# Kernel optimization log

Measured on AMD Instinct MI355X. Metric: run time of the kernel, lower is better.

## Reference

```python
import jax, jax.numpy as jnp
import numpy as np

N, D = 4096, 512
W_L2, W_TOPO = 1.0, 1.0
BIG = jnp.float32(1e30)


def setup_inputs() -> dict:
    key = jax.random.key(0)
    k1, k2 = jax.random.split(key)
    x_1 = jax.random.normal(k1, (N, D), dtype=jnp.float32)
    x_2 = jax.random.normal(k2, (N, D), dtype=jnp.float32)
    return {"x_1": x_1, "x_2": x_2}


def _pdist(x):
    # Euclidean pairwise distances [n, n]; diagonal set to BIG so it is never
    # selected as an MST edge and sqrt(0) never appears in the grad path.
    sq = jnp.sum(x * x, axis=1)
    d2 = sq[:, None] + sq[None, :] - 2.0 * (x @ x.T)
    d2 = jnp.maximum(d2, 1e-12)
    n = x.shape[0]
    d2 = jnp.where(jnp.eye(n, dtype=bool), BIG, d2)
    return jnp.sqrt(d2)


def _h0_deaths(dist):
    # H0 persistence of the Vietoris-Rips filtration == MST edge weights
    # (births are all 0). Prim's algorithm via lax.scan, O(n^2).
    n = dist.shape[0]
    in_tree0 = jnp.zeros(n, dtype=bool).at[0].set(True)

    def step(carry, _):
        min_dist, in_tree = carry  # min_dist[k] = min edge from tree to k
        md = jnp.where(in_tree, BIG, min_dist)
        j = jnp.argmin(md)
        w = md[j]  # weight of the MST edge added this step = an H0 death
        min_dist = jnp.minimum(min_dist, dist[j])
        in_tree = in_tree.at[j].set(True)
        return (min_dist, in_tree), w

    (_, _), deaths = jax.lax.scan(step, (dist[0], in_tree0), None, length=n - 1)
    return deaths  # [n-1]


def _wasserstein1(d1, d2):
    # 1-Wasserstein between two H0 diagrams {(0, death_i)} with L_inf ground
    # metric and diagonal projections allowed. Equal-cardinality diagrams on
    # the birth=0 axis: match sorted deaths, per-pair cost is the cheaper of
    # direct matching |a-b| or routing both points to the diagonal (a+b)/2.
    a = jnp.sort(d1)
    b = jnp.sort(d2)
    cost = jnp.minimum(jnp.abs(a - b), 0.5 * (a + b))
    return jnp.sum(cost)


def reference(x_1, x_2):
    representation_loss = jnp.mean((x_1 - x_2) ** 2)
    deaths_1 = _h0_deaths(_pdist(x_1))
    deaths_2 = _h0_deaths(_pdist(x_2))
    topological_loss = _wasserstein1(deaths_1, deaths_2)
    return W_L2 * representation_loss + W_TOPO * topological_loss
```

## Files before the change

### kernel.cpp

```cpp
#include <hip/hip_runtime.h>

#define N 4096
#define D 512
#define BIG 1e30f
#define CMAX 2048
#define CMAX2 1024
#define CMAX3 512
#define NW (N / 32)

typedef unsigned long long u64;
typedef unsigned short u16;
typedef _Float16 f16x8 __attribute__((ext_vector_type(8)));
typedef float floatx4 __attribute__((ext_vector_type(4)));

__global__ __launch_bounds__(256) void prep_kernel(const float* __restrict__ x1,
                                                   const float* __restrict__ x2,
                                                   u16* __restrict__ h1,
                                                   u16* __restrict__ h2,
                                                   float* __restrict__ sq,
                                                   float* __restrict__ accumArr,
                                                   int* __restrict__ comp,
                                                   u64* __restrict__ compBest,
                                                   int* __restrict__ comp_c,
                                                   int* __restrict__ doneFlag) {
    const int tid = blockIdx.x * 256 + threadIdx.x;
    if (tid < 2 * N) {
        comp[tid] = tid & (N - 1);
        compBest[tid] = ~0ull;
    }
    if (tid < 2 * CMAX) comp_c[tid] = tid & (CMAX - 1);
    if (tid == 0) doneFlag[0] = 0;

    const int wave = threadIdx.x >> 6, lane = threadIdx.x & 63;
    const int row = blockIdx.x * 4 + wave;
    const float4* r1 = (const float4*)(x1 + (size_t)row * D);
    const float4* r2 = (const float4*)(x2 + (size_t)row * D);
    float4 a0 = r1[lane * 2], a1 = r1[lane * 2 + 1];
    float4 b0 = r2[lane * 2], b1 = r2[lane * 2 + 1];
    ushort4* o1 = (ushort4*)(h1 + (size_t)row * D + lane * 8);
    ushort4* o2 = (ushort4*)(h2 + (size_t)row * D + lane * 8);
    o1[0] = make_ushort4(__builtin_bit_cast(u16, (_Float16)a0.x), __builtin_bit_cast(u16, (_Float16)a0.y),
                         __builtin_bit_cast(u16, (_Float16)a0.z), __builtin_bit_cast(u16, (_Float16)a0.w));
    o1[1] = make_ushort4(__builtin_bit_cast(u16, (_Float16)a1.x), __builtin_bit_cast(u16, (_Float16)a1.y),
                         __builtin_bit_cast(u16, (_Float16)a1.z), __builtin_bit_cast(u16, (_Float16)a1.w));
    o2[0] = make_ushort4(__builtin_bit_cast(u16, (_Float16)b0.x), __builtin_bit_cast(u16, (_Float16)b0.y),
                         __builtin_bit_cast(u16, (_Float16)b0.z), __builtin_bit_cast(u16, (_Float16)b0.w));
    o2[1] = make_ushort4(__builtin_bit_cast(u16, (_Float16)b1.x), __builtin_bit_cast(u16, (_Float16)b1.y),
                         __builtin_bit_cast(u16, (_Float16)b1.z), __builtin_bit_cast(u16, (_Float16)b1.w));
    float s1 = 0.f, s2 = 0.f, sr = 0.f;
    float av[8] = {a0.x, a0.y, a0.z, a0.w, a1.x, a1.y, a1.z, a1.w};
    float bv[8] = {b0.x, b0.y, b0.z, b0.w, b1.x, b1.y, b1.z, b1.w};
#pragma unroll
    for (int e = 0; e < 8; ++e) {
        s1 = fmaf(av[e], av[e], s1);
        s2 = fmaf(bv[e], bv[e], s2);
        float d = av[e] - bv[e];
        sr = fmaf(d, d, sr);
    }
#pragma unroll
    for (int off = 32; off > 0; off >>= 1) {
        s1 += __shfl_down(s1, off, 64);
        s2 += __shfl_down(s2, off, 64);
        sr += __shfl_down(sr, off, 64);
    }
    __shared__ float wsr[4];
    if (lane == 0) {
        sq[row] = s1;
        sq[N + row] = s2;
        wsr[wave] = sr;
    }
    __syncthreads();
    if (threadIdx.x == 0)
        accumArr[blockIdx.x] = wsr[0] + wsr[1] + wsr[2] + wsr[3];
}

#define BM 128
#define BN 128
#define BK 32
#define NB (N / BM)
#define NPAIR (NB * (NB + 1) / 2)
#define NT (D / BK)

__global__ __launch_bounds__(256) void gemm_dist_sym_kernel(const u16* __restrict__ h1,
                                                            const u16* __restrict__ h2,
                                                            const float* __restrict__ sqn,
                                                            float* __restrict__ dist1,
                                                            float* __restrict__ dist2,
                                                            u64* __restrict__ compBest) {
    const int m = blockIdx.z;
    const u16* H = m ? h2 : h1;
    const float* SQ = sqn + (size_t)m * N;
    float* dist = m ? dist2 : dist1;
    u64* cb = compBest + (size_t)m * N;

    const int t = blockIdx.x;
    int by = (int)((65.0f - sqrtf(4225.0f - 8.0f * (float)t)) * 0.5f);
    while (by > 0 && by * 32 - by * (by - 1) / 2 > t) --by;
    while ((by + 1) * 32 - (by + 1) * by / 2 <= t) ++by;
    const int bx = by + (t - (by * 32 - by * (by - 1) / 2));
    const bool diag = (by == bx);

    __shared__ u16 SH[4 * BM * BK];
    u16* A0 = SH;
    u16* B0 = SH + BM * BK;
    u16* A1 = SH + 2 * BM * BK;
    u16* B1 = SH + 3 * BM * BK;

    const int tid = threadIdx.x;
    const int wave = tid >> 6, lane = tid & 63;
    const int wm = wave >> 1, wn = wave & 1;
    const int row0 = by * BM, col0 = bx * BN;

    floatx4 acc[4][4] = {};

    const int srow = lane >> 2;
    const int scol = (lane & 3) * 8;

#define STAGE(AB, BB, K0)                                                                      \
    {                                                                                          \
        _Pragma("unroll") for (int i_ = 0; i_ < 2; ++i_) {                                     \
            const int rb_ = wave * 32 + i_ * 16;                                               \
            const u16* ga_ = H + (size_t)(row0 + rb_ + srow) * D + (K0) + scol;                \
            __builtin_amdgcn_global_load_lds(                                                  \
                (const __attribute__((address_space(1))) unsigned int*)ga_,                    \
                (__attribute__((address_space(3))) unsigned int*)&(AB)[rb_ * BK], 16, 0, 0);   \
            if (!diag) {                                                                       \
                const u16* gb_ = H + (size_t)(col0 + rb_ + srow) * D + (K0) + scol;            \
                __builtin_amdgcn_global_load_lds(                                              \
                    (const __attribute__((address_space(1))) unsigned int*)gb_,                \
                    (__attribute__((address_space(3))) unsigned int*)&(BB)[rb_ * BK], 16, 0, 0); \
            }                                                                                  \
        }                                                                                      \
    }

    STAGE(A0, B0, 0);
    __syncthreads();

    const int fo = (lane >> 4) * 8;
    const int fm = lane & 15;
#pragma unroll 2
    for (int kt = 0; kt < NT; ++kt) {
        u16* Ac = (kt & 1) ? A1 : A0;
        u16* Bc = (kt & 1) ? B1 : B0;
        if (kt + 1 < NT) {
            u16* An = (kt & 1) ? A0 : A1;
            u16* Bn = (kt & 1) ? B0 : B1;
            STAGE(An, Bn, (kt + 1) * BK);
        }
        const u16* Bs = diag ? Ac : Bc;
        f16x8 a8[4], b8[4];
#pragma unroll
        for (int s = 0; s < 4; ++s) {
            a8[s] = *(const f16x8*)&Ac[(wm * 64 + s * 16 + fm) * BK + fo];
            b8[s] = *(const f16x8*)&Bs[(wn * 64 + s * 16 + fm) * BK + fo];
        }
#pragma unroll
        for (int i = 0; i < 4; ++i)
#pragma unroll
            for (int j = 0; j < 4; ++j)
                acc[i][j] = __builtin_amdgcn_mfma_f32_16x16x32_f16(a8[i], b8[j], acc[i][j], 0, 0, 0);
        __syncthreads();
    }
#undef STAGE

    float* Cs = (float*)SH + wave * 1024;

    const int lr = lane & 15;
    const int lq = lane >> 4;
    float sc[4];
#pragma unroll
    for (int ns = 0; ns < 4; ++ns) sc[ns] = SQ[col0 + wn * 64 + ns * 16 + lr];
    u64 colBest[4] = {~0ull, ~0ull, ~0ull, ~0ull};
#pragma unroll
    for (int ms = 0; ms < 4; ++ms) {
        const int rb = row0 + wm * 64 + ms * 16 + lq * 4;
        float srow_[4];
#pragma unroll
        for (int r = 0; r < 4; ++r) srow_[r] = SQ[rb + r];
#pragma unroll
        for (int r = 0; r < 4; ++r) {
            const int row = rb + r;
            float dval[4];
#pragma unroll
            for (int ns = 0; ns < 4; ++ns) {
                const int col = col0 + wn * 64 + ns * 16 + lr;
                float d2 = srow_[r] + sc[ns] - 2.0f * acc[ms][ns][r];
                dval[ns] = (row == col) ? BIG : sqrtf(fmaxf(d2, 1e-12f));
            }
            float vmin = fminf(fminf(dval[0], dval[1]), fminf(dval[2], dval[3]));
            int nsel = (dval[0] == vmin) ? 0 : (dval[1] == vmin) ? 1 : (dval[2] == vmin) ? 2 : 3;
            u64 pmin = (((u64)__float_as_uint(vmin)) << 32) | (unsigned)(col0 + wn * 64 + nsel * 16 + lr);
#pragma unroll
            for (int msk = 1; msk < 16; msk <<= 1) {
                u64 o = __shfl_xor(pmin, msk, 64);
                pmin = o < pmin ? o : pmin;
            }
            if (lr == 0) atomicMin(&cb[row], pmin);
            if (!diag) {
#pragma unroll
                for (int ns = 0; ns < 4; ++ns) {
                    u64 p = (((u64)__float_as_uint(dval[ns])) << 32) | (unsigned)row;
                    colBest[ns] = p < colBest[ns] ? p : colBest[ns];
                }
            }
#pragma unroll
            for (int ns = 0; ns < 4; ++ns)
                Cs[(lq * 4 + r) * 64 + ns * 16 + lr] = dval[ns];
        }
#pragma unroll
        for (int p = 0; p < 4; ++p) {
            float4 v4 = *(float4*)&Cs[p * 256 + lane * 4];
            const int gr = row0 + wm * 64 + ms * 16 + p * 4 + (lane >> 4);
            const int gc = col0 + wn * 64 + (lane & 15) * 4;
            *(float4*)&dist[(size_t)gr * N + gc] = v4;
        }
    }
    if (!diag) {
#pragma unroll
        for (int ns = 0; ns < 4; ++ns) {
            u64 b = colBest[ns];
            u64 o = __shfl_xor(b, 16, 64);
            b = o < b ? o : b;
            o = __shfl_xor(b, 32, 64);
            b = o < b ? o : b;
            if (lq == 0) atomicMin(&cb[col0 + wn * 64 + ns * 16 + lr], b);
        }
    }
}

__global__ __launch_bounds__(1024) void merge1i_kernel(int* __restrict__ comp,
                                                       u64* __restrict__ compBest,
                                                       float* __restrict__ deaths,
                                                       int* __restrict__ cnt,
                                                       int* __restrict__ numComp,
                                                       int* __restrict__ numC1,
                                                       unsigned* __restrict__ distc_u) {
    const int t = threadIdx.x;
    if (blockIdx.x >= 2) {
        const size_t idx = (size_t)(blockIdx.x - 2) * 1024 + t;
        uint4 v = make_uint4(0x7f800000u, 0x7f800000u, 0x7f800000u, 0x7f800000u);
        ((uint4*)distc_u)[idx] = v;
        ((uint4*)distc_u)[idx + 1048576] = v;
        return;
    }
    const int m = blockIdx.x;
    int* cp = comp + (size_t)m * N;
    u64* cb = compBest + (size_t)m * N;
    float* dth = deaths + (size_t)m * N;

    __shared__ int pa[N];
    __shared__ int pb[N];
    __shared__ unsigned flagbits[NW];
    __shared__ int wpc[NW];
    __shared__ int done;

    if (t == 0) cnt[m] = 0;
    __syncthreads();

    for (int c = t; c < N; c += 1024) {
        u64 best = cb[c];
        int p = c;
        if (best != ~0ull) {
            int j = (int)(unsigned)best;
            int c2 = cp[j];
            u64 best2 = cb[c2];
            int j2 = (int)(unsigned)best2;
            bool mutual = (cp[j2] == c);
            if (!(mutual && c < c2)) {
                p = c2;
                int idx = atomicAdd(cnt + m, 1);
                dth[idx] = __uint_as_float((unsigned)(best >> 32));
            }
        }
        pa[c] = p;
    }

    int* A = pa;
    int* B = pb;
    while (true) {
        __syncthreads();
        if (t == 0) done = 1;
        __syncthreads();
        bool ch = false;
        for (int c = t; c < N; c += 1024) {
            int g = A[A[c]];
            B[c] = g;
            ch |= (g != A[c]);
        }
        if (ch) done = 0;
        __syncthreads();
        int* tmp = A; A = B; B = tmp;
        if (done) break;
    }

    for (int w = t; w < NW; w += 1024) flagbits[w] = 0u;
    __syncthreads();
    for (int i = t; i < N; i += 1024)
        atomicOr(&flagbits[A[i] >> 5], 1u << (A[i] & 31));
    __syncthreads();
    if (t < NW) wpc[t] = __popc(flagbits[t]);
    __syncthreads();
    for (int off = 1; off < NW; off <<= 1) {
        int v = 0;
        if (t < NW) v = wpc[t] + ((t >= off) ? wpc[t - off] : 0);
        __syncthreads();
        if (t < NW) wpc[t] = v;
        __syncthreads();
    }
    for (int i = t; i < N; i += 1024) {
        int root = A[i];
        int w = root >> 5, b = root & 31;
        int base = w ? wpc[w - 1] : 0;
        unsigned mask = b ? ((1u << b) - 1u) : 0u;
        cp[i] = base + __popc(flagbits[w] & mask);
    }
    for (int c = t; c < N; c += 1024) cb[c] = ~0ull;
    if (t == 0) {
        int C1 = wpc[NW - 1];
        numC1[m] = C1;
        numComp[m] = C1;
    }
}

__global__ __launch_bounds__(256) void rowatomic_kernel(const float* __restrict__ dist1,
                                                        const float* __restrict__ dist2,
                                                        const int* __restrict__ comp,
                                                        unsigned* __restrict__ distc_u) {
    const int m = blockIdx.y;
    const float* dist = m ? dist2 : dist1;
    const int* cp = comp + (size_t)m * N;
    const int i = blockIdx.x;
    const float4* row4 = (const float4*)(dist + (size_t)i * N);
    const int4* cp4 = (const int4*)cp;
    __shared__ unsigned bins[CMAX];
    const int t = threadIdx.x;
    for (int b = t; b < CMAX; b += 256) bins[b] = 0x7f800000u;
    __syncthreads();
    const int q0 = (i >> 7) << 5;
    for (int q = q0 + t; q < N / 4; q += 256) {
        float4 v = row4[q];
        int4 cj = cp4[q];
        atomicMin(&bins[cj.x], __float_as_uint(v.x));
        atomicMin(&bins[cj.y], __float_as_uint(v.y));
        atomicMin(&bins[cj.z], __float_as_uint(v.z));
        atomicMin(&bins[cj.w], __float_as_uint(v.w));
    }
    __syncthreads();
    unsigned* drow = distc_u + ((size_t)m * CMAX + cp[i]) * CMAX;
    for (int b = t; b < CMAX; b += 256) {
        unsigned v = bins[b];
        if (v != 0x7f800000u) atomicMin(&drow[b], v);
    }
}

#define CT 64
#define NCT (CMAX / CT)
#define NPAIRC (NCT * (NCT + 1) / 2)
__global__ __launch_bounds__(256) void symscan_kernel(unsigned* __restrict__ distc_u,
                                                      u64* __restrict__ compBest,
                                                      const int* __restrict__ numComp,
                                                      const int* __restrict__ numC1,
                                                      unsigned* __restrict__ distc2_u) {
    const int tid = threadIdx.x;
    if (blockIdx.x >= NPAIRC) {
        const size_t base = ((size_t)blockIdx.y * 256 + (blockIdx.x - NPAIRC)) * 256 + tid;
        uint4 v = make_uint4(0x7f800000u, 0x7f800000u, 0x7f800000u, 0x7f800000u);
#pragma unroll
        for (int k = 0; k < 4; ++k)
            ((uint4*)distc2_u)[base + (size_t)k * 131072] = v;
        return;
    }
    const int m = blockIdx.y;
    if (numComp[m] <= 1) return;
    const int C1 = numC1[m];
    const int t = blockIdx.x;
    int a = (int)((65.0f - sqrtf(4225.0f - 8.0f * (float)t)) * 0.5f);
    while (a > 0 && a * 32 - a * (a - 1) / 2 > t) --a;
    while ((a + 1) * 32 - (a + 1) * a / 2 <= t) ++a;
    const int b = a + (t - (a * 32 - a * (a - 1) / 2));
    if (a * CT >= C1 || b * CT >= C1) return;

    unsigned* Dm = distc_u + (size_t)m * CMAX * CMAX;
    unsigned* P = Dm + (size_t)(a * CT) * CMAX + b * CT;
    unsigned* Q = Dm + (size_t)(b * CT) * CMAX + a * CT;
    u64* cb = compBest + (size_t)m * N;

    __shared__ float L[CT][CT + 1];
    __shared__ float M[CT][CT + 1];
#pragma unroll
    for (int e0 = 0; e0 < 4; ++e0) {
        int e = e0 * 256 + tid;
        int r = e >> 4, c4 = (e & 15) << 2;
        float4 v = *(const float4*)&Q[(size_t)r * CMAX + c4];
        L[r][c4] = v.x; L[r][c4 + 1] = v.y; L[r][c4 + 2] = v.z; L[r][c4 + 3] = v.w;
    }
    __syncthreads();
#pragma unroll
    for (int e0 = 0; e0 < 4; ++e0) {
        int e = e0 * 256 + tid;
        int r = e >> 4, c4 = (e & 15) << 2;
        float4 v = *(const float4*)&P[(size_t)r * CMAX + c4];
        float4 f;
        f.x = fminf(v.x, L[c4 + 0][r]);
        f.y = fminf(v.y, L[c4 + 1][r]);
        f.z = fminf(v.z, L[c4 + 2][r]);
        f.w = fminf(v.w, L[c4 + 3][r]);
        *(float4*)&P[(size_t)r * CMAX + c4] = f;
        M[r][c4] = f.x; M[r][c4 + 1] = f.y; M[r][c4 + 2] = f.z; M[r][c4 + 3] = f.w;
    }
    __syncthreads();

    {
        const int rloc = tid >> 2;
        const int r = a * CT + rloc;
        const int c0 = (tid & 3) * 16;
        u64 best = ~0ull;
#pragma unroll
        for (int c = 0; c < 16; ++c) {
            const int j = b * CT + c0 + c;
            const unsigned bits = __float_as_uint(M[rloc][c0 + c]);
            if (j < C1 && j != r && bits < 0x7f800000u) {
                u64 p = (((u64)bits) << 32) | (unsigned)j;
                best = p < best ? p : best;
            }
        }
        u64 o = __shfl_xor(best, 1, 64); best = o < best ? o : best;
        o = __shfl_xor(best, 2, 64); best = o < best ? o : best;
        if ((tid & 3) == 0 && r < C1 && best != ~0ull) atomicMin(&cb[r], best);
    }

    if (a == b) return;

    {
        const int rloc = tid >> 2;
        const int r = b * CT + rloc;
        const int c0 = (tid & 3) * 16;
        u64 best = ~0ull;
#pragma unroll
        for (int c = 0; c < 16; ++c) {
            const int j = a * CT + c0 + c;
            const unsigned bits = __float_as_uint(M[c0 + c][rloc]);
            if (j < C1 && bits < 0x7f800000u) {
                u64 p = (((u64)bits) << 32) | (unsigned)j;
                best = p < best ? p : best;
            }
        }
        u64 o = __shfl_xor(best, 1, 64); best = o < best ? o : best;
        o = __shfl_xor(best, 2, 64); best = o < best ? o : best;
        if ((tid & 3) == 0 && r < C1 && best != ~0ull) atomicMin(&cb[r], best);
    }

#pragma unroll
    for (int e0 = 0; e0 < 4; ++e0) {
        int e = e0 * 256 + tid;
        int r = e >> 4, c4 = (e & 15) << 2;
        float4 f;
        f.x = M[c4 + 0][r];
        f.y = M[c4 + 1][r];
        f.z = M[c4 + 2][r];
        f.w = M[c4 + 3][r];
        *(float4*)&Q[(size_t)r * CMAX + c4] = f;
    }
}

__global__ __launch_bounds__(1024) void merge2_kernel(int* __restrict__ comp_c,
                                                      u64* __restrict__ compBest,
                                                      float* __restrict__ deaths,
                                                      int* __restrict__ cnt,
                                                      int* __restrict__ numComp,
                                                      const int* __restrict__ numC1,
                                                      int* __restrict__ numC2,
                                                      int* __restrict__ comp_c2) {
    const int m = blockIdx.x;
    const int t = threadIdx.x;
    const int C1 = numC1[m];
    int* cc2i = comp_c2 + (size_t)m * CMAX2;
    for (int c = t; c < CMAX2; c += 1024) cc2i[c] = c;
    if (numComp[m] <= 1) {
        if (t == 0) numC2[m] = numComp[m];
        return;
    }
    int* cc = comp_c + (size_t)m * CMAX;
    u64* cb = compBest + (size_t)m * N;
    float* dth = deaths + (size_t)m * N;

    __shared__ int pa[CMAX];
    __shared__ int pb[CMAX];
    __shared__ unsigned flagbits[CMAX / 32];
    __shared__ int wpc[CMAX / 32];
    __shared__ int done;

    for (int c = t; c < C1; c += 1024) {
        u64 best = cb[c];
        int p = c;
        if (best != ~0ull) {
            int j = (int)(unsigned)best;
            int c2 = cc[j];
            u64 best2 = cb[c2];
            int j2 = (int)(unsigned)best2;
            bool mutual = (cc[j2] == c);
            if (!(mutual && c < c2)) {
                p = c2;
                int idx = atomicAdd(cnt + m, 1);
                dth[idx] = __uint_as_float((unsigned)(best >> 32));
            }
        }
        pa[c] = p;
    }

    int* A = pa;
    int* B = pb;
    while (true) {
        __syncthreads();
        if (t == 0) done = 1;
        __syncthreads();
        bool ch = false;
        for (int c = t; c < C1; c += 1024) {
            int g = A[A[c]];
            B[c] = g;
            ch |= (g != A[c]);
        }
        if (ch) done = 0;
        __syncthreads();
        int* tmp = A; A = B; B = tmp;
        if (done) break;
    }

    for (int w = t; w < CMAX / 32; w += 1024) flagbits[w] = 0u;
    __syncthreads();
    for (int j = t; j < C1; j += 1024)
        atomicOr(&flagbits[A[j] >> 5], 1u << (A[j] & 31));
    __syncthreads();
    if (t < CMAX / 32) wpc[t] = __popc(flagbits[t]);
    __syncthreads();
    for (int off = 1; off < CMAX / 32; off <<= 1) {
        int v = 0;
        if (t < CMAX / 32) v = wpc[t] + ((t >= off) ? wpc[t - off] : 0);
        __syncthreads();
        if (t < CMAX / 32) wpc[t] = v;
        __syncthreads();
    }
    for (int j = t; j < C1; j += 1024) {
        int root = A[j];
        int w = root >> 5, b = root & 31;
        int base = w ? wpc[w - 1] : 0;
        unsigned mask = b ? ((1u << b) - 1u) : 0u;
        cc[j] = base + __popc(flagbits[w] & mask);
    }
    for (int c = t; c < C1; c += 1024) cb[c] = ~0ull;
    if (t == 0) {
        int C2 = wpc[CMAX / 32 - 1];
        numC2[m] = C2;
        numComp[m] = C2;
    }
}

__global__ __launch_bounds__(256) void rowatomic2_kernel(const float* __restrict__ distc,
                                                         const int* __restrict__ comp_c,
                                                         const int* __restrict__ numComp,
                                                         const int* __restrict__ numC1,
                                                         unsigned* __restrict__ distc2_u) {
    const int m = blockIdx.y;
    if (numComp[m] <= 1) return;
    const int C1 = numC1[m];
    const int r = blockIdx.x;
    if (r >= C1) return;
    const int* cc = comp_c + (size_t)m * CMAX;
    const float* row = distc + ((size_t)m * CMAX + r) * CMAX;
    __shared__ unsigned bins[CMAX2];
    const int t = threadIdx.x;
    for (int b = t; b < CMAX2; b += 256) bins[b] = 0x7f800000u;
    __syncthreads();
    for (int j = t; j < C1; j += 256)
        atomicMin(&bins[cc[j]], __float_as_uint(row[j]));
    __syncthreads();
    unsigned* drow = distc2_u + ((size_t)m * CMAX2 + cc[r]) * CMAX2;
    for (int b = t; b < CMAX2; b += 256) {
        unsigned v = bins[b];
        if (v != 0x7f800000u) atomicMin(&drow[b], v);
    }
}

__global__ __launch_bounds__(256) void scan3_kernel(const float* __restrict__ distc2,
                                                    const int* __restrict__ comp_c2,
                                                    u64* __restrict__ compBest,
                                                    const int* __restrict__ numComp,
                                                    const int* __restrict__ numC2,
                                                    unsigned* __restrict__ distc3_u) {
    const int t = threadIdx.x;
    if (blockIdx.x >= 2 * CMAX2) {
        const size_t idx = (size_t)(blockIdx.x - 2 * CMAX2) * 256 + t;
        uint4 v = make_uint4(0x7f800000u, 0x7f800000u, 0x7f800000u, 0x7f800000u);
        ((uint4*)distc3_u)[idx] = v;
        ((uint4*)distc3_u)[idx + 65536] = v;
        return;
    }
    const int m = blockIdx.x >> 10;
    if (numComp[m] <= 1) return;
    const int C2 = numC2[m];
    const int r = blockIdx.x & (CMAX2 - 1);
    if (r >= C2) return;
    const int* cc = comp_c2 + (size_t)m * CMAX2;
    u64* cb = compBest + (size_t)m * N;
    const int myc = cc[r];
    const float4* row4 = (const float4*)(distc2 + ((size_t)m * CMAX2 + r) * CMAX2);
    const int4* cc4 = (const int4*)cc;
    float4 v = row4[t];
    int4 cj = cc4[t];
    int j0 = t * 4;
    u64 p0 = (j0 + 0 < C2 && cj.x != myc) ? ((((u64)__float_as_uint(v.x)) << 32) | (unsigned)(j0 + 0)) : ~0ull;
    u64 p1 = (j0 + 1 < C2 && cj.y != myc) ? ((((u64)__float_as_uint(v.y)) << 32) | (unsigned)(j0 + 1)) : ~0ull;
    u64 p2 = (j0 + 2 < C2 && cj.z != myc) ? ((((u64)__float_as_uint(v.z)) << 32) | (unsigned)(j0 + 2)) : ~0ull;
    u64 p3 = (j0 + 3 < C2 && cj.w != myc) ? ((((u64)__float_as_uint(v.w)) << 32) | (unsigned)(j0 + 3)) : ~0ull;
    u64 q0 = p0 < p1 ? p0 : p1;
    u64 q1 = p2 < p3 ? p2 : p3;
    u64 best = q0 < q1 ? q0 : q1;
#pragma unroll
    for (int off = 32; off > 0; off >>= 1) {
        u64 o = __shfl_down(best, off, 64);
        best = o < best ? o : best;
    }
    if ((t & 63) == 0) atomicMin(cb + myc, best);
}

__global__ __launch_bounds__(1024) void merge3_kernel(int* __restrict__ comp_c2,
                                                      u64* __restrict__ compBest,
                                                      float* __restrict__ deaths,
                                                      int* __restrict__ cnt,
                                                      int* __restrict__ numComp,
                                                      const int* __restrict__ numC2,
                                                      int* __restrict__ numC3) {
    const int m = blockIdx.x;
    const int t = threadIdx.x;
    if (numComp[m] <= 1) {
        if (t == 0) numC3[m] = numComp[m];
        return;
    }
    const int C2 = numC2[m];
    int* cc = comp_c2 + (size_t)m * CMAX2;
    u64* cb = compBest + (size_t)m * N;
    float* dth = deaths + (size_t)m * N;

    __shared__ int pa[CMAX2];
    __shared__ int pb[CMAX2];
    __shared__ unsigned flagbits[CMAX2 / 32];
    __shared__ int wpc[CMAX2 / 32];
    __shared__ int done;

    for (int c = t; c < C2; c += 1024) {
        u64 best = cb[c];
        int p = c;
        if (best != ~0ull) {
            int j = (int)(unsigned)best;
            int c2 = cc[j];
            u64 best2 = cb[c2];
            int j2 = (int)(unsigned)best2;
            bool mutual = (cc[j2] == c);
            if (!(mutual && c < c2)) {
                p = c2;
                int idx = atomicAdd(cnt + m, 1);
                dth[idx] = __uint_as_float((unsigned)(best >> 32));
            }
        }
        pa[c] = p;
    }

    int* A = pa;
    int* B = pb;
    while (true) {
        __syncthreads();
        if (t == 0) done = 1;
        __syncthreads();
        bool ch = false;
        for (int c = t; c < C2; c += 1024) {
            int g = A[A[c]];
            B[c] = g;
            ch |= (g != A[c]);
        }
        if (ch) done = 0;
        __syncthreads();
        int* tmp = A; A = B; B = tmp;
        if (done) break;
    }

    for (int w = t; w < CMAX2 / 32; w += 1024) flagbits[w] = 0u;
    __syncthreads();
    for (int j = t; j < C2; j += 1024)
        atomicOr(&flagbits[A[j] >> 5], 1u << (A[j] & 31));
    __syncthreads();
    if (t < CMAX2 / 32) wpc[t] = __popc(flagbits[t]);
    __syncthreads();
    for (int off = 1; off < CMAX2 / 32; off <<= 1) {
        int v = 0;
        if (t < CMAX2 / 32) v = wpc[t] + ((t >= off) ? wpc[t - off] : 0);
        __syncthreads();
        if (t < CMAX2 / 32) wpc[t] = v;
        __syncthreads();
    }
    for (int j = t; j < C2; j += 1024) {
        int root = A[j];
        int w = root >> 5, b = root & 31;
        int base = w ? wpc[w - 1] : 0;
        unsigned mask = b ? ((1u << b) - 1u) : 0u;
        cc[j] = base + __popc(flagbits[w] & mask);
    }
    for (int c = t; c < C2; c += 1024) cb[c] = ~0ull;
    if (t == 0) {
        int C3 = wpc[CMAX2 / 32 - 1];
        numC3[m] = C3;
        numComp[m] = C3;
    }
}

__global__ __launch_bounds__(256) void rowatomic3_kernel(const float* __restrict__ distc2,
                                                         const int* __restrict__ comp_c2,
                                                         const int* __restrict__ numComp,
                                                         const int* __restrict__ numC2,
                                                         unsigned* __restrict__ distc3_u) {
    const int m = blockIdx.y;
    if (numComp[m] <= 1) return;
    const int C2 = numC2[m];
    const int r = blockIdx.x;
    if (r >= C2) return;
    const int* cc = comp_c2 + (size_t)m * CMAX2;
    const float* row = distc2 + ((size_t)m * CMAX2 + r) * CMAX2;
    __shared__ unsigned bins[CMAX3];
    const int t = threadIdx.x;
    for (int b = t; b < CMAX3; b += 256) bins[b] = 0x7f800000u;
    __syncthreads();
    for (int j = t; j < C2; j += 256)
        atomicMin(&bins[cc[j]], __float_as_uint(row[j]));
    __syncthreads();
    unsigned* drow = distc3_u + ((size_t)m * CMAX3 + cc[r]) * CMAX3;
    for (int b = t; b < CMAX3; b += 256) {
        unsigned v = bins[b];
        if (v != 0x7f800000u) atomicMin(&drow[b], v);
    }
}

__global__ __launch_bounds__(1024) void finish_kernel(const float* __restrict__ distc3,
                                                      float* __restrict__ deaths,
                                                      int* __restrict__ cnt,
                                                      int* __restrict__ numComp,
                                                      const int* __restrict__ numC3,
                                                      const float* __restrict__ accumArr,
                                                      int* __restrict__ doneFlag,
                                                      float* __restrict__ out) {
    const int m = blockIdx.x;
    int nc = numComp[m];
    const int C3 = numC3[m];
    const float* Dm = distc3 + (size_t)m * CMAX3 * CMAX3;
    float* dth = deaths + (size_t)m * N;
    const int t = threadIdx.x;
    const int wave = t >> 6, lane = t & 63;
    __shared__ int comp[CMAX3];
    __shared__ u64 cb[CMAX3];
    __shared__ int pa[CMAX3];
    __shared__ int pb[CMAX3];
    __shared__ unsigned flags[CMAX3 / 32];
    __shared__ int done, ncs, lastf;
    __shared__ float s[N];
    __shared__ float wsum[16];
    __shared__ float rsum[16];

    if (nc > 1) {
        for (int c = t; c < C3; c += 1024) {
            comp[c] = c;
            cb[c] = ~0ull;
        }
        __syncthreads();

        for (int round = 0; round < 10 && nc > 1; ++round) {
            for (int r = wave; r < C3; r += 16) {
                const int myc = comp[r];
                const float* row = Dm + (size_t)r * CMAX3;
                u64 best = ~0ull;
                for (int j = lane; j < C3; j += 64) {
                    if (comp[j] != myc) {
                        u64 p = (((u64)__float_as_uint(row[j])) << 32) | (unsigned)j;
                        best = p < best ? p : best;
                    }
                }
#pragma unroll
                for (int off = 32; off > 0; off >>= 1) {
                    u64 o = __shfl_down(best, off, 64);
                    best = o < best ? o : best;
                }
                if (lane == 0) atomicMin(&cb[myc], best);
            }
            __syncthreads();
            for (int c = t; c < C3; c += 1024) {
                u64 best = cb[c];
                int p = c;
                if (best != ~0ull) {
                    int j = (int)(unsigned)best;
                    int c2 = comp[j];
                    u64 best2 = cb[c2];
                    int j2 = (int)(unsigned)best2;
                    bool mutual = (comp[j2] == c);
                    if (!(mutual && c < c2)) {
                        p = c2;
                        int idx = atomicAdd(cnt + m, 1);
                        dth[idx] = __uint_as_float((unsigned)(best >> 32));
                    }
                }
                pa[c] = p;
            }
            int* A = pa; int* B = pb;
            while (true) {
                __syncthreads();
                if (t == 0) done = 1;
                __syncthreads();
                bool ch = false;
                for (int c = t; c < C3; c += 1024) {
                    int g = A[A[c]];
                    B[c] = g;
                    ch |= (g != A[c]);
                }
                if (ch) done = 0;
                __syncthreads();
                int* tmp = A; A = B; B = tmp;
                if (done) break;
            }
            for (int w = t; w < CMAX3 / 32; w += 1024) flags[w] = 0u;
            __syncthreads();
            for (int j = t; j < C3; j += 1024) {
                int root = A[comp[j]];
                comp[j] = root;
                atomicOr(&flags[root >> 5], 1u << (root & 31));
            }
            for (int c = t; c < C3; c += 1024) cb[c] = ~0ull;
            __syncthreads();
            if (t == 0) {
                int sacc = 0;
                for (int w = 0; w < CMAX3 / 32; ++w) sacc += __popc(flags[w]);
                ncs = sacc;
            }
            __syncthreads();
            nc = ncs;
        }
        if (t == 0) numComp[m] = nc;
    }
    __syncthreads();

    const int t4 = t << 2;
    float v0, v1, v2, v3;
    {
        float4 l4 = *(const float4*)&dth[t4];
        v0 = l4.x; v1 = l4.y; v2 = l4.z; v3 = l4.w;
        if (t == 1023) v3 = BIG;
    }
#define CSWAP(a, b, up)                         \
    {                                           \
        float mn_ = fminf(a, b), mx_ = fmaxf(a, b); \
        a = (up) ? mn_ : mx_;                   \
        b = (up) ? mx_ : mn_;                   \
    }
    for (int k = 2; k <= N; k <<= 1) {
        for (int jj = k >> 1; jj > 0; jj >>= 1) {
            if (jj >= 256) {
                s[t4] = v0; s[t4 + 1] = v1; s[t4 + 2] = v2; s[t4 + 3] = v3;
                __syncthreads();
                const bool up = ((t4 & k) == 0);
                const bool lower = ((t4 & jj) == 0);
                const bool mk = (up == lower);
                float o0 = s[t4 ^ jj], o1 = s[(t4 + 1) ^ jj];
                float o2 = s[(t4 + 2) ^ jj], o3 = s[(t4 + 3) ^ jj];
                v0 = mk ? fminf(v0, o0) : fmaxf(v0, o0);
                v1 = mk ? fminf(v1, o1) : fmaxf(v1, o1);
                v2 = mk ? fminf(v2, o2) : fmaxf(v2, o2);
                v3 = mk ? fminf(v3, o3) : fmaxf(v3, o3);
                __syncthreads();
            } else if (jj >= 4) {
                const int sl = jj >> 2;
                const bool up = ((t4 & k) == 0);
                const bool lower = ((lane & sl) == 0);
                const bool mk = (up == lower);
                float o0 = __shfl_xor(v0, sl, 64);
                float o1 = __shfl_xor(v1, sl, 64);
                float o2 = __shfl_xor(v2, sl, 64);
                float o3 = __shfl_xor(v3, sl, 64);
                v0 = mk ? fminf(v0, o0) : fmaxf(v0, o0);
                v1 = mk ? fminf(v1, o1) : fmaxf(v1, o1);
                v2 = mk ? fminf(v2, o2) : fmaxf(v2, o2);
                v3 = mk ? fminf(v3, o3) : fmaxf(v3, o3);
            } else if (jj == 2) {
                const bool up = ((t4 & k) == 0);
                CSWAP(v0, v2, up);
                CSWAP(v1, v3, up);
            } else {
                const bool u01 = ((t4 & k) == 0);
                const bool u23 = (((t4 + 2) & k) == 0);
                CSWAP(v0, v1, u01);
                CSWAP(v2, v3, u23);
            }
        }
    }
#undef CSWAP
    *(float4*)&dth[t4] = make_float4(v0, v1, v2, v3);

    __threadfence();
    __syncthreads();
    if (t == 0) lastf = (atomicAdd(doneFlag, 1) == 1) ? 1 : 0;
    __syncthreads();
    if (!lastf) return;
    __threadfence();
    const float* s1 = deaths;
    const float* s2 = deaths + N;
    float sum = 0.f;
    for (int i = t; i < N - 1; i += 1024) {
        float a = s1[i], b = s2[i];
        sum += fminf(fabsf(a - b), 0.5f * (a + b));
    }
    float ra = accumArr[t];
#pragma unroll
    for (int off = 32; off > 0; off >>= 1) {
        sum += __shfl_down(sum, off, 64);
        ra += __shfl_down(ra, off, 64);
    }
    if (lane == 0) { wsum[wave] = sum; rsum[wave] = ra; }
    __syncthreads();
    if (t == 0) {
        float tot = 0.f, rt = 0.f;
        for (int k = 0; k < 16; ++k) { tot += wsum[k]; rt += rsum[k]; }
        out[0] = rt * (1.0f / ((float)N * (float)D)) + tot;
    }
}

extern "C" void kernel_launch(void* const* d_in, const int* in_sizes, int n_in,
                              void* d_out, int out_size, void* d_ws, size_t ws_size,
                              hipStream_t stream) {
    const float* x1 = (const float*)d_in[0];
    const float* x2 = (const float*)d_in[1];
    float* out = (float*)d_out;
    float* ws = (float*)d_ws;

    const size_t nn = (size_t)N * N;
    const size_t cc2 = (size_t)CMAX * CMAX;

    float* dist1 = ws;
    float* dist2 = ws + nn;
    float* distc = ws + 2 * nn;
    u16* h1 = (u16*)distc;
    u16* h2 = h1 + (size_t)N * D;
    u64* compBest = (u64*)(distc + 2 * cc2);
    int* comp      = (int*)(compBest + 2 * N);
    int* comp_c    = comp + 2 * N;
    float* deaths  = (float*)(comp_c + 2 * CMAX);
    int* cnt       = (int*)(deaths + 2 * N);
    int* numComp   = cnt + 2;
    int* numC1     = numComp + 2;
    int* numC2     = numC1 + 2;
    int* numC3     = numC2 + 2;
    int* doneFlag  = numC3 + 2;
    float* sq      = (float*)(doneFlag + 2);
    float* accumArr = sq + 2 * N;
    float* distc2  = dist1;
    int* comp_c2   = (int*)(distc2 + 2 * (size_t)CMAX2 * CMAX2);
    float* distc3  = distc;

    prep_kernel<<<N / 4, 256, 0, stream>>>(x1, x2, h1, h2, sq, accumArr, comp, compBest,
                                           comp_c, doneFlag);
    gemm_dist_sym_kernel<<<dim3(NPAIR, 1, 2), 256, 0, stream>>>(h1, h2, sq, dist1, dist2, compBest);
    merge1i_kernel<<<2 + 1024, 1024, 0, stream>>>(comp, compBest, deaths, cnt, numComp, numC1,
                                                  (unsigned*)distc);
    rowatomic_kernel<<<dim3(N, 2), 256, 0, stream>>>(dist1, dist2, comp, (unsigned*)distc);
    symscan_kernel<<<dim3(NPAIRC + 256, 2), 256, 0, stream>>>((unsigned*)distc, compBest,
                                                              numComp, numC1, (unsigned*)distc2);
    merge2_kernel<<<2, 1024, 0, stream>>>(comp_c, compBest, deaths, cnt, numComp, numC1, numC2,
                                          comp_c2);
    rowatomic2_kernel<<<dim3(CMAX, 2), 256, 0, stream>>>(distc, comp_c, numComp, numC1,
                                                         (unsigned*)distc2);
    scan3_kernel<<<2 * CMAX2 + 256, 256, 0, stream>>>(distc2, comp_c2, compBest, numComp, numC2,
                                                      (unsigned*)distc3);
    merge3_kernel<<<2, 1024, 0, stream>>>(comp_c2, compBest, deaths, cnt, numComp, numC2, numC3);
    rowatomic3_kernel<<<dim3(CMAX2, 2), 256, 0, stream>>>(distc2, comp_c2, numComp, numC2,
                                                          (unsigned*)distc3);
    finish_kernel<<<2, 1024, 0, stream>>>(distc3, deaths, cnt, numComp, numC3,
                                          accumArr, doneFlag, out);
}
```

Baseline: 227.8 us.

## Group rows by component to replace global atomics and swizzle GEMM LDS layout

Adds a counting sort in merge1i that builds per-component row lists. The new rowgroup kernel gives each block one component: it reduces all of that component's rows into shared bins, then writes the contracted-distance row directly. This removes the separate INF-fill of distc and the global atomicMin traffic, but load balance now depends on component sizes. The GEMM also XOR-swizzles the LDS column offsets used in staging and fragment reads, to reduce bank conflicts.

Result: slower. 544.6 us (+139.1%).

```diff
diff --git a/kernel.cpp b/kernel.cpp
--- a/kernel.cpp
+++ b/kernel.cpp
@@ -114,7 +114,7 @@
     floatx4 acc[4][4] = {};
 
     const int srow = lane >> 2;
-    const int scol = (lane & 3) * 8;
+    const int scol = (((lane & 3) ^ ((lane >> 3) & 3))) * 8;
 
 #define STAGE(AB, BB, K0)                                                                      \
     {                                                                                          \
@@ -136,7 +136,7 @@
     STAGE(A0, B0, 0);
     __syncthreads();
 
-    const int fo = (lane >> 4) * 8;
+    const int cs = (((lane >> 4) ^ ((lane >> 1) & 3))) * 8;
     const int fm = lane & 15;
 #pragma unroll 2
     for (int kt = 0; kt < NT; ++kt) {
@@ -151,8 +151,8 @@
         f16x8 a8[4], b8[4];
 #pragma unroll
         for (int s = 0; s < 4; ++s) {
-            a8[s] = *(const f16x8*)&Ac[(wm * 64 + s * 16 + fm) * BK + fo];
-            b8[s] = *(const f16x8*)&Bs[(wn * 64 + s * 16 + fm) * BK + fo];
+            a8[s] = *(const f16x8*)&Ac[(wm * 64 + s * 16 + fm) * BK + cs];
+            b8[s] = *(const f16x8*)&Bs[(wn * 64 + s * 16 + fm) * BK + cs];
         }
 #pragma unroll
         for (int i = 0; i < 4; ++i)
@@ -234,19 +234,15 @@
                                                        int* __restrict__ cnt,
                                                        int* __restrict__ numComp,
                                                        int* __restrict__ numC1,
-                                                       unsigned* __restrict__ distc_u) {
+                                                       int* __restrict__ rowStart,
+                                                       int* __restrict__ rowlist) {
     const int t = threadIdx.x;
-    if (blockIdx.x >= 2) {
-        const size_t idx = (size_t)(blockIdx.x - 2) * 1024 + t;
-        uint4 v = make_uint4(0x7f800000u, 0x7f800000u, 0x7f800000u, 0x7f800000u);
-        ((uint4*)distc_u)[idx] = v;
-        ((uint4*)distc_u)[idx + 1048576] = v;
-        return;
-    }
     const int m = blockIdx.x;
     int* cp = comp + (size_t)m * N;
     u64* cb = compBest + (size_t)m * N;
     float* dth = deaths + (size_t)m * N;
+    int* rsG = rowStart + (size_t)m * (CMAX + 1);
+    int* rlG = rowlist + (size_t)m * N;
 
     __shared__ int pa[N];
     __shared__ int pb[N];
@@ -320,37 +316,71 @@
         numC1[m] = C1;
         numComp[m] = C1;
     }
-}
-
-__global__ __launch_bounds__(256) void rowatomic_kernel(const float* __restrict__ dist1,
-                                                        const float* __restrict__ dist2,
-                                                        const int* __restrict__ comp,
-                                                        unsigned* __restrict__ distc_u) {
+    __syncthreads();
+
+    int* X = pb;
+    int* Y = pa;
+    for (int c = t; c < CMAX; c += 1024) X[c] = 0;
+    __syncthreads();
+    for (int i = t; i < N; i += 1024) atomicAdd(&X[cp[i]], 1);
+    __syncthreads();
+    for (int off = 1; off < CMAX; off <<= 1) {
+        for (int c = t; c < CMAX; c += 1024)
+            Y[c] = X[c] + ((c >= off) ? X[c - off] : 0);
+        __syncthreads();
+        int* tmp = X; X = Y; Y = tmp;
+    }
+    for (int c = t; c < CMAX; c += 1024) {
+        int ex = c ? X[c - 1] : 0;
+        Y[c] = ex;
+        rsG[c] = ex;
+    }
+    if (t == 0) rsG[CMAX] = N;
+    __syncthreads();
+    for (int i = t; i < N; i += 1024) {
+        int pos = atomicAdd(&Y[cp[i]], 1);
+        rlG[pos] = i;
+    }
+}
+
+__global__ __launch_bounds__(256) void rowgroup_kernel(const float* __restrict__ dist1,
+                                                       const float* __restrict__ dist2,
+                                                       const int* __restrict__ comp,
+                                                       const int* __restrict__ rowlist,
+                                                       const int* __restrict__ rowStart,
+                                                       const int* __restrict__ numC1,
+                                                       unsigned* __restrict__ distc_u) {
     const int m = blockIdx.y;
+    const int C1 = numC1[m];
+    const int r = blockIdx.x;
+    if (r >= C1) return;
+    const int cend = (C1 + 63) & ~63;
     const float* dist = m ? dist2 : dist1;
     const int* cp = comp + (size_t)m * N;
-    const int i = blockIdx.x;
-    const float4* row4 = (const float4*)(dist + (size_t)i * N);
     const int4* cp4 = (const int4*)cp;
+    const int* rl = rowlist + (size_t)m * N;
+    const int* rs = rowStart + (size_t)m * (CMAX + 1);
+    const int s0 = rs[r], s1 = rs[r + 1];
     __shared__ unsigned bins[CMAX];
     const int t = threadIdx.x;
-    for (int b = t; b < CMAX; b += 256) bins[b] = 0x7f800000u;
-    __syncthreads();
-    const int q0 = (i >> 7) << 5;
-    for (int q = q0 + t; q < N / 4; q += 256) {
-        float4 v = row4[q];
-        int4 cj = cp4[q];
-        atomicMin(&bins[cj.x], __float_as_uint(v.x));
-        atomicMin(&bins[cj.y], __float_as_uint(v.y));
-        atomicMin(&bins[cj.z], __float_as_uint(v.z));
-        atomicMin(&bins[cj.w], __float_as_uint(v.w));
-    }
-    __syncthreads();
-    unsigned* drow = distc_u + ((size_t)m * CMAX + cp[i]) * CMAX;
-    for (int b = t; b < CMAX; b += 256) {
-        unsigned v = bins[b];
-        if (v != 0x7f800000u) atomicMin(&drow[b], v);
-    }
+    for (int b = t; b < cend; b += 256) bins[b] = 0x7f800000u;
+    __syncthreads();
+    for (int ri = s0; ri < s1; ++ri) {
+        const int i = rl[ri];
+        const float4* row4 = (const float4*)(dist + (size_t)i * N);
+        const int q0 = (i >> 7) << 5;
+        for (int q = q0 + t; q < N / 4; q += 256) {
+            float4 v = row4[q];
+            int4 cj = cp4[q];
+            atomicMin(&bins[cj.x], __float_as_uint(v.x));
+            atomicMin(&bins[cj.y], __float_as_uint(v.y));
+            atomicMin(&bins[cj.z], __float_as_uint(v.z));
+            atomicMin(&bins[cj.w], __float_as_uint(v.w));
+        }
+    }
+    __syncthreads();
+    unsigned* drow = distc_u + ((size_t)m * CMAX + r) * CMAX;
+    for (int b = t; b < cend; b += 256) drow[b] = bins[b];
 }
 
 #define CT 64
@@ -955,6 +985,8 @@
     int* doneFlag  = numC3 + 2;
     float* sq      = (float*)(doneFlag + 2);
     float* accumArr = sq + 2 * N;
+    int* rowStart  = (int*)(accumArr + 1024);
+    int* rowlist   = rowStart + 2 * (CMAX + 1);
     float* distc2  = dist1;
     int* comp_c2   = (int*)(distc2 + 2 * (size_t)CMAX2 * CMAX2);
     float* distc3  = distc;
@@ -962,9 +994,10 @@
     prep_kernel<<<N / 4, 256, 0, stream>>>(x1, x2, h1, h2, sq, accumArr, comp, compBest,
                                            comp_c, doneFlag);
     gemm_dist_sym_kernel<<<dim3(NPAIR, 1, 2), 256, 0, stream>>>(h1, h2, sq, dist1, dist2, compBest);
-    merge1i_kernel<<<2 + 1024, 1024, 0, stream>>>(comp, compBest, deaths, cnt, numComp, numC1,
-                                                  (unsigned*)distc);
-    rowatomic_kernel<<<dim3(N, 2), 256, 0, stream>>>(dist1, dist2, comp, (unsigned*)distc);
+    merge1i_kernel<<<2, 1024, 0, stream>>>(comp, compBest, deaths, cnt, numComp, numC1,
+                                           rowStart, rowlist);
+    rowgroup_kernel<<<dim3(CMAX, 2), 256, 0, stream>>>(dist1, dist2, comp, rowlist, rowStart,
+                                                       numC1, (unsigned*)distc);
     symscan_kernel<<<dim3(NPAIRC + 256, 2), 256, 0, stream>>>((unsigned*)distc, compBest,
                                                               numComp, numC1, (unsigned*)distc2);
     merge2_kernel<<<2, 1024, 0, stream>>>(comp_c, compBest, deaths, cnt, numComp, numC1, numC2,
```
